# Performance work log

Hardware: AMD Instinct MI355X
Metric: run time of the kernel (lower is better)

The kernel has to match this reference:

```python
import jax, jax.numpy as jnp
import numpy as np

N = 100000
E = 1600000
H = 64      # hidden_size
NH = 8      # num_heads
DH = H // NH  # per-head dim (heads are the LAST axis, as in the torch code)


def _lin(x, W, b):
    return x @ W + b


def setup_inputs() -> dict:
    key = jax.random.key(0)
    ks = jax.random.split(key, 18)
    s = 0.05
    inp = {
        "h_x": jax.random.normal(ks[0], (N, H), jnp.float32),
        "h_e": jax.random.normal(ks[1], (E, H), jnp.float32),
        "row": jax.random.randint(ks[2], (E,), 0, N, jnp.int32),  # dst node of each nonzero
        "col": jax.random.randint(ks[3], (E,), 0, N, jnp.int32),  # src node of each nonzero
    }
    names = ["q", "k", "v", "e", "oh", "oe"]
    for i, nm in enumerate(names):
        inp["W" + nm] = jax.random.normal(ks[4 + 2 * i], (H, H), jnp.float32) * s
        inp["b" + nm] = jax.random.normal(ks[5 + 2 * i], (H,), jnp.float32) * s
    return inp


def reference(h_x, h_e, row, col, Wq, bq, Wk, bk, Wv, bv, We, be, Woh, boh, Woe, boe):
    n = h_x.shape[0]
    m = h_e.shape[0]
    q = _lin(h_x, Wq, bq).reshape(n, DH, NH)
    k = _lin(h_x, Wk, bk).reshape(n, DH, NH)
    v = _lin(h_x, Wv, bv).reshape(n, DH, NH)
    e = _lin(h_e, We, be).reshape(m, DH, NH)

    # SDDMM: per-nonzero (i=row, j=col), per-head dot of q[i] and k[j]  -> (E, NH)
    scores = (q[row] * k[col]).sum(axis=1) / jnp.sqrt(jnp.float32(DH))

    # edge gating: e.sum over dh axis -> (E, NH)
    e_gate = e.sum(axis=1)
    scores = scores * e_gate

    # oe branch (uses pre-softmax gated scores)
    oe_feat = scores[:, None, :] * e          # (E, DH, NH)
    oe = _lin(oe_feat.reshape(m, H), Woe, boe)

    # sparse softmax over dim=1 (per destination row), per head
    mx = jax.ops.segment_max(scores, row, num_segments=n)      # (N, NH)
    ex = jnp.exp(scores - mx[row])
    den = jax.ops.segment_sum(ex, row, num_segments=n)         # (N, NH)
    sm = ex / den[row]                                          # (E, NH)

    # bSpMM: h_out[i,:,h] = sum_{e: row[e]=i} sm[e,h] * v[col[e],:,h]
    h_out = jax.ops.segment_sum(sm[:, None, :] * v[col], row, num_segments=n)
    oh = _lin(h_out.reshape(n, H), Woh, boh)
    return (oh, oe)
```

## Files before the change

### kernel.cpp

```cpp
#include <hip/hip_runtime.h>

typedef __attribute__((ext_vector_type(8))) short bf16x8;
typedef __attribute__((ext_vector_type(4))) float f32x4;

__device__ __forceinline__ float bf2f(unsigned short h) {
  return __uint_as_float(((unsigned)h) << 16);
}
__device__ __forceinline__ unsigned cvtpk(float a, float b) {
  unsigned r;
  asm("v_cvt_pk_bf16_f32 %0, %1, %2" : "=v"(r) : "v"(a), "v"(b));
  return r;
}
__device__ __forceinline__ unsigned short f2bf(float f) {
  return (unsigned short)(cvtpk(f, f) & 0xffffu);
}
__device__ __forceinline__ bf16x8 pack8(f32x4 x0, f32x4 x1) {
  union { bf16x8 v; unsigned u[4]; } z;
  z.u[0] = cvtpk(x0[0], x0[1]);
  z.u[1] = cvtpk(x0[2], x0[3]);
  z.u[2] = cvtpk(x1[0], x1[1]);
  z.u[3] = cvtpk(x1[2], x1[3]);
  return z.v;
}

template<bool IN_BF16, bool OUT_BF16>
__global__ void __launch_bounds__(256) gemm64_kernel(const void* __restrict__ Ain,
    const float* __restrict__ W, const float* __restrict__ bias,
    void* __restrict__ Out, int M) {
  const int tid = threadIdx.x;
  const int l = tid & 63;
  const int g = l >> 4;
  const int n15 = l & 15;

  bf16x8 bfrag[4][2];
  float bv[4];
#pragma unroll
  for (int nb = 0; nb < 4; ++nb) {
    bv[nb] = bias[nb * 16 + n15];
#pragma unroll
    for (int kb = 0; kb < 2; ++kb)
#pragma unroll
      for (int j = 0; j < 8; ++j)
        bfrag[nb][kb][j] = (short)f2bf(W[(kb * 32 + g * 8 + j) * 64 + nb * 16 + n15]);
  }

  int wid = (blockIdx.x * blockDim.x + tid) >> 6;
  int nw = (gridDim.x * blockDim.x) >> 6;
  int ntiles = (M + 15) >> 4;
  for (int t = wid; t < ntiles; t += nw) {
    int m0 = t << 4;
    int arow = m0 + n15;
    bf16x8 a0, a1;
    if (arow < M) {
      if constexpr (IN_BF16) {
        const unsigned short* ap = (const unsigned short*)Ain + (size_t)arow * 64 + g * 8;
        a0 = *(const bf16x8*)ap;
        a1 = *(const bf16x8*)(ap + 32);
      } else {
        const float* ap = (const float*)Ain + (size_t)arow * 64 + g * 8;
        a0 = pack8(*(const f32x4*)ap, *(const f32x4*)(ap + 4));
        a1 = pack8(*(const f32x4*)(ap + 32), *(const f32x4*)(ap + 36));
      }
    } else {
#pragma unroll
      for (int j = 0; j < 8; ++j) { a0[j] = 0; a1[j] = 0; }
    }
    f32x4 acc[4];
#pragma unroll
    for (int nb = 0; nb < 4; ++nb) {
      acc[nb] = (f32x4){bv[nb], bv[nb], bv[nb], bv[nb]};
      acc[nb] = __builtin_amdgcn_mfma_f32_16x16x32_bf16(a0, bfrag[nb][0], acc[nb], 0, 0, 0);
      acc[nb] = __builtin_amdgcn_mfma_f32_16x16x32_bf16(a1, bfrag[nb][1], acc[nb], 0, 0, 0);
    }
#pragma unroll
    for (int nb = 0; nb < 4; ++nb)
#pragma unroll
      for (int r = 0; r < 4; ++r) {
        int orow = m0 + g * 4 + r;
        if (orow < M) {
          float val = acc[nb][r];
          size_t oidx = (size_t)orow * 64 + nb * 16 + n15;
          if constexpr (OUT_BF16) ((unsigned short*)Out)[oidx] = f2bf(val);
          else                    ((float*)Out)[oidx] = val;
        }
      }
  }
}

__global__ void __launch_bounds__(256) qkv3_kernel(const float* __restrict__ hx,
    const float* __restrict__ Wq, const float* __restrict__ bq,
    const float* __restrict__ Wk, const float* __restrict__ bk,
    const float* __restrict__ Wv, const float* __restrict__ bv,
    unsigned short* __restrict__ q, unsigned short* __restrict__ k,
    unsigned short* __restrict__ v, int M) {
  const int tid = threadIdx.x;
  const int l = tid & 63;
  const int g = l >> 4;
  const int n15 = l & 15;
  const float* Ws[3] = {Wq, Wk, Wv};
  const float* bs[3] = {bq, bk, bv};
  unsigned short* outs[3] = {q, k, v};

  bf16x8 bfrag[3][4][2];
  float bvv[3][4];
#pragma unroll
  for (int w = 0; w < 3; ++w)
#pragma unroll
    for (int nb = 0; nb < 4; ++nb) {
      bvv[w][nb] = bs[w][nb * 16 + n15];
#pragma unroll
      for (int kb = 0; kb < 2; ++kb)
#pragma unroll
        for (int j = 0; j < 8; ++j)
          bfrag[w][nb][kb][j] = (short)f2bf(Ws[w][(kb * 32 + g * 8 + j) * 64 + nb * 16 + n15]);
    }

  int wid = (blockIdx.x * blockDim.x + tid) >> 6;
  int nw = (gridDim.x * blockDim.x) >> 6;
  int ntiles = (M + 15) >> 4;
  for (int t = wid; t < ntiles; t += nw) {
    int m0 = t << 4;
    int arow = m0 + n15;
    bf16x8 a0, a1;
    if (arow < M) {
      const float* ap = hx + (size_t)arow * 64 + g * 8;
      a0 = pack8(*(const f32x4*)ap, *(const f32x4*)(ap + 4));
      a1 = pack8(*(const f32x4*)(ap + 32), *(const f32x4*)(ap + 36));
    } else {
#pragma unroll
      for (int j = 0; j < 8; ++j) { a0[j] = 0; a1[j] = 0; }
    }
#pragma unroll
    for (int w = 0; w < 3; ++w) {
      f32x4 acc[4];
#pragma unroll
      for (int nb = 0; nb < 4; ++nb) {
        acc[nb] = (f32x4){bvv[w][nb], bvv[w][nb], bvv[w][nb], bvv[w][nb]};
        acc[nb] = __builtin_amdgcn_mfma_f32_16x16x32_bf16(a0, bfrag[w][nb][0], acc[nb], 0, 0, 0);
        acc[nb] = __builtin_amdgcn_mfma_f32_16x16x32_bf16(a1, bfrag[w][nb][1], acc[nb], 0, 0, 0);
      }
#pragma unroll
      for (int nb = 0; nb < 4; ++nb)
#pragma unroll
        for (int r = 0; r < 4; ++r) {
          int orow = m0 + g * 4 + r;
          if (orow < M)
            outs[w][(size_t)orow * 64 + nb * 16 + n15] = f2bf(acc[nb][r]);
        }
    }
  }
}

__global__ void __launch_bounds__(256) edge_fused_kernel(
    const float* __restrict__ he,
    const int* __restrict__ rowi, const int* __restrict__ coli,
    const int* __restrict__ eslot,
    const unsigned short* __restrict__ qb, const unsigned short* __restrict__ kbuf,
    const float* __restrict__ We, const float* __restrict__ be,
    const float* __restrict__ Woe, const float* __restrict__ boe,
    float* __restrict__ oe, float* __restrict__ escores, int E) {
  const int tid = threadIdx.x;
  const int wv = tid >> 6;
  const int l = tid & 63;
  const int g = l >> 4;
  const int n15 = l & 15;
  const int h = n15 & 7;

  __shared__ float s_lds[4][160];
  __shared__ unsigned short feat_lds[4][16 * 72];

  bf16x8 bfE[4][2], bfO[4][2];
  float beV[4], boV[4];
#pragma unroll
  for (int nb = 0; nb < 4; ++nb) {
    beV[nb] = be[nb * 16 + n15];
    boV[nb] = boe[nb * 16 + n15];
#pragma unroll
    for (int kb = 0; kb < 2; ++kb)
#pragma unroll
      for (int j = 0; j < 8; ++j) {
        bfE[nb][kb][j] = (short)f2bf(We[(kb * 32 + g * 8 + j) * 64 + nb * 16 + n15]);
        bfO[nb][kb][j] = (short)f2bf(Woe[(kb * 32 + g * 8 + j) * 64 + nb * 16 + n15]);
      }
  }

  const int ntiles = (E + 15) >> 4;
  const int nit = (ntiles + 3) >> 2;
  const int stride = gridDim.x;

  int it = blockIdx.x;
  if (it >= nit) return;

  f32x4 h0, h1, h2, h3;
  int rq, rc, sl;
  {
    int m0 = ((it << 2) + wv) << 4;
    int es = min(m0 + n15, E - 1);
    const float* ap = he + (size_t)es * 64 + g * 8;
    h0 = *(const f32x4*)ap;       h1 = *(const f32x4*)(ap + 4);
    h2 = *(const f32x4*)(ap + 32); h3 = *(const f32x4*)(ap + 36);
    rq = rowi[es]; rc = coli[es]; sl = eslot[es];
  }

  while (true) {
    const int m0 = ((it << 2) + wv) << 4;
    const int arow = m0 + n15;

    const unsigned short* qp = qb + (size_t)rq * 64 + g * 16;
    const unsigned short* kp = kbuf + (size_t)rc * 64 + g * 16;
    bf16x8 qv0 = *(const bf16x8*)qp, qv1 = *(const bf16x8*)(qp + 8);
    bf16x8 kv0 = *(const bf16x8*)kp, kv1 = *(const bf16x8*)(kp + 8);

    const int itn = it + stride;
    const bool more = itn < nit;
    f32x4 nh0 = h0, nh1 = h1, nh2 = h2, nh3 = h3;
    int nrq = rq, nrc = rc, nsl = sl;
    if (more) {
      int m0n = ((itn << 2) + wv) << 4;
      int es = min(m0n + n15, E - 1);
      const float* ap = he + (size_t)es * 64 + g * 8;
      nh0 = *(const f32x4*)ap;       nh1 = *(const f32x4*)(ap + 4);
      nh2 = *(const f32x4*)(ap + 32); nh3 = *(const f32x4*)(ap + 36);
      nrq = rowi[es]; nrc = coli[es]; nsl = eslot[es];
    }

    bf16x8 a0 = pack8(h0, h1), a1 = pack8(h2, h3);
    if (arow >= E) {
#pragma unroll
      for (int j = 0; j < 8; ++j) { a0[j] = 0; a1[j] = 0; }
    }
    f32x4 acc[4];
#pragma unroll
    for (int nb = 0; nb < 4; ++nb) {
      acc[nb] = (f32x4){beV[nb], beV[nb], beV[nb], beV[nb]};
      acc[nb] = __builtin_amdgcn_mfma_f32_16x16x32_bf16(a0, bfE[nb][0], acc[nb], 0, 0, 0);
      acc[nb] = __builtin_amdgcn_mfma_f32_16x16x32_bf16(a1, bfE[nb][1], acc[nb], 0, 0, 0);
    }
    float gc[4];
#pragma unroll
    for (int r = 0; r < 4; ++r) {
      float s = acc[0][r] + acc[1][r] + acc[2][r] + acc[3][r];
      s += __shfl_xor(s, 8, 64);
      gc[r] = s * 0.35355339059327373f;
    }
    float p[8];
#pragma unroll
    for (int j = 0; j < 8; ++j)
      p[j] = bf2f((unsigned short)qv0[j]) * bf2f((unsigned short)kv0[j])
           + bf2f((unsigned short)qv1[j]) * bf2f((unsigned short)kv1[j]);
#pragma unroll
    for (int j = 0; j < 8; ++j) {
      p[j] += __shfl_xor(p[j], 16, 64);
      p[j] += __shfl_xor(p[j], 32, 64);
    }
    if (l < 16) {
      float2* sp = (float2*)&s_lds[wv][n15 * 10];
#pragma unroll
      for (int j = 0; j < 4; ++j) sp[j] = make_float2(p[2 * j], p[2 * j + 1]);
    }
    float srow[4];
#pragma unroll
    for (int r = 0; r < 4; ++r)
      srow[r] = s_lds[wv][(g * 4 + r) * 10 + h] * gc[r];
#pragma unroll
    for (int r = 0; r < 4; ++r) {
      int orow = m0 + g * 4 + r;
      int slot = __shfl(sl, g * 4 + r, 64);
      if (n15 < 8 && orow < E) escores[(size_t)slot * 8 + n15] = srow[r];
    }
#pragma unroll
    for (int nb = 0; nb < 4; ++nb)
#pragma unroll
      for (int r = 0; r < 4; ++r)
        feat_lds[wv][(g * 4 + r) * 72 + nb * 16 + n15] = f2bf(srow[r] * acc[nb][r]);
    const unsigned short* fpt = &feat_lds[wv][n15 * 72 + g * 8];
    a0 = *(const bf16x8*)fpt;
    a1 = *(const bf16x8*)(fpt + 32);
#pragma unroll
    for (int nb = 0; nb < 4; ++nb) {
      f32x4 a2 = (f32x4){boV[nb], boV[nb], boV[nb], boV[nb]};
      a2 = __builtin_amdgcn_mfma_f32_16x16x32_bf16(a0, bfO[nb][0], a2, 0, 0, 0);
      a2 = __builtin_amdgcn_mfma_f32_16x16x32_bf16(a1, bfO[nb][1], a2, 0, 0, 0);
#pragma unroll
      for (int r = 0; r < 4; ++r) {
        int orow = m0 + g * 4 + r;
        if (orow < E) oe[(size_t)orow * 64 + nb * 16 + n15] = a2[r];
      }
    }

    if (!more) break;
    h0 = nh0; h1 = nh1; h2 = nh2; h3 = nh3;
    rq = nrq; rc = nrc; sl = nsl;
    it = itn;
  }
}

__global__ void zero_kernel(int* __restrict__ p, int n) {
  int i = blockIdx.x * blockDim.x + threadIdx.x;
  if (i < n) p[i] = 0;
}

__global__ void hist_kernel(const int* __restrict__ row, int* __restrict__ deg, int E) {
  int gid = blockIdx.x * blockDim.x + threadIdx.x;
  if (gid < E) atomicAdd(&deg[row[gid]], 1);
}

#define SCAN_B 256
#define SCAN_E 8
__global__ void scan1_kernel(const int* __restrict__ deg, int* __restrict__ rowptr,
                             int* __restrict__ blksum, int n) {
  __shared__ int sh[SCAN_B];
  int base = blockIdx.x * (SCAN_B * SCAN_E) + threadIdx.x * SCAN_E;
  int v[SCAN_E];
  int s = 0;
#pragma unroll
  for (int j = 0; j < SCAN_E; ++j) {
    v[j] = (base + j < n) ? deg[base + j] : 0;
    s += v[j];
  }
  sh[threadIdx.x] = s;
  __syncthreads();
  for (int off = 1; off < SCAN_B; off <<= 1) {
    int t = (threadIdx.x >= off) ? sh[threadIdx.x - off] : 0;
    __syncthreads();
    sh[threadIdx.x] += t;
    __syncthreads();
  }
  if (threadIdx.x == SCAN_B - 1) blksum[blockIdx.x] = sh[SCAN_B - 1];
  int run = sh[threadIdx.x] - s;
#pragma unroll
  for (int j = 0; j < SCAN_E; ++j) {
    if (base + j < n) rowptr[base + j] = run;
    run += v[j];
  }
}

__global__ void scan2_kernel(int* __restrict__ blksum, int nb) {
  __shared__ int sh[SCAN_B];
  int v = (threadIdx.x < nb) ? blksum[threadIdx.x] : 0;
  sh[threadIdx.x] = v;
  __syncthreads();
  for (int off = 1; off < SCAN_B; off <<= 1) {
    int t = (threadIdx.x >= off) ? sh[threadIdx.x - off] : 0;
    __syncthreads();
    sh[threadIdx.x] += t;
    __syncthreads();
  }
  if (threadIdx.x < nb) blksum[threadIdx.x] = sh[threadIdx.x] - v;
}

__global__ void scan3_kernel(int* __restrict__ rowptr, int* __restrict__ cursor,
                             const int* __restrict__ blksum, int n) {
  int i = blockIdx.x * blockDim.x + threadIdx.x;
  if (i >= n) return;
  int v = rowptr[i] + blksum[i / (SCAN_B * SCAN_E)];
  rowptr[i] = v;
  cursor[i] = v;
}

__global__ void scatter_kernel(const int* __restrict__ row, const int* __restrict__ col,
                               int* __restrict__ cursor, int* __restrict__ eslot,
                               int* __restrict__ ecol, int E) {
  int gid = blockIdx.x * blockDim.x + threadIdx.x;
  if (gid >= E) return;
  int r = row[gid];
  int slot = atomicAdd(&cursor[r], 1);
  eslot[gid] = slot;
  ecol[slot] = col[gid];
}

__global__ void __launch_bounds__(256) row_attn_kernel(const float* __restrict__ escores,
    const int* __restrict__ rowptr, const int* __restrict__ deg,
    const int* __restrict__ ecol,
    const unsigned short* __restrict__ vb, float* __restrict__ hout, int n) {
  int gid = blockIdx.x * blockDim.x + threadIdx.x;
  int r = gid >> 6, lane = threadIdx.x & 63;
  if (r >= n) return;
  int start = rowptr[r], dg = deg[r];
  int h = lane & 7;
  float den = 0.f, acc = 0.f;
#pragma unroll 4
  for (int i = 0; i < dg; ++i) {
    int c = ecol[start + i];
    float ex = __expf(escores[(size_t)(start + i) * 8 + h]);
    float vv = bf2f(vb[(size_t)c * 64 + lane]);
    den += ex;
    acc += ex * vv;
  }
  hout[(size_t)r * 64 + lane] = (dg > 0) ? acc / den : 0.f;
}

extern "C" void kernel_launch(void* const* d_in, const int* in_sizes, int n_in,
                              void* d_out, int out_size, void* d_ws, size_t ws_size,
                              hipStream_t stream) {
  const float* hx  = (const float*)d_in[0];
  const float* he  = (const float*)d_in[1];
  const int*   row = (const int*)d_in[2];
  const int*   col = (const int*)d_in[3];
  const float* Wq = (const float*)d_in[4],  *bq = (const float*)d_in[5];
  const float* Wk = (const float*)d_in[6],  *bk = (const float*)d_in[7];
  const float* Wv = (const float*)d_in[8],  *bv = (const float*)d_in[9];
  const float* We = (const float*)d_in[10], *be = (const float*)d_in[11];
  const float* Woh = (const float*)d_in[12], *boh = (const float*)d_in[13];
  const float* Woe = (const float*)d_in[14], *boe = (const float*)d_in[15];

  const int n = in_sizes[0] / 64;
  const int E = in_sizes[2];

  float* out = (float*)d_out;
  float* oh = out;
  float* oe = out + (size_t)n * 64;

  unsigned short* qb   = (unsigned short*)d_ws;
  unsigned short* kb   = qb + (size_t)n * 64;
  unsigned short* vbuf = kb + (size_t)n * 64;
  float* escores = (float*)(vbuf + (size_t)n * 64);
  float* hout    = escores + (size_t)E * 8;

  int* deg    = (int*)(hout + (size_t)n * 64);
  int* rowptr = deg + n;
  int* cursor = rowptr + n;
  int* blksum = cursor + n;
  int* eslot  = blksum + 256;
  int* ecol   = eslot + (size_t)E;

  const int nb_scan = (n + SCAN_B * SCAN_E - 1) / (SCAN_B * SCAN_E);

  zero_kernel<<<(n + 255) / 256, 256, 0, stream>>>(deg, n);
  hist_kernel<<<(E + 255) / 256, 256, 0, stream>>>(row, deg, E);
  scan1_kernel<<<nb_scan, SCAN_B, 0, stream>>>(deg, rowptr, blksum, n);
  scan2_kernel<<<1, SCAN_B, 0, stream>>>(blksum, nb_scan);
  scan3_kernel<<<(n + 255) / 256, 256, 0, stream>>>(rowptr, cursor, blksum, n);
  scatter_kernel<<<(E + 255) / 256, 256, 0, stream>>>(row, col, cursor, eslot, ecol, E);

  qkv3_kernel<<<512, 256, 0, stream>>>(hx, Wq, bq, Wk, bk, Wv, bv, qb, kb, vbuf, n);
  edge_fused_kernel<<<2048, 256, 0, stream>>>(he, row, col, eslot, qb, kb, We, be,
                                              Woe, boe, oe, escores, E);

  row_attn_kernel<<<(n + 3) / 4, 256, 0, stream>>>(escores, rowptr, deg, ecol,
                                                   vbuf, hout, n);
  gemm64_kernel<false, false><<<512, 256, 0, stream>>>(hout, Woh, boh, oh, n);
}
```

Baseline: 550.8 us.

## Process two edge tiles per iteration and parallelize row attention across edges

The edge kernel now handles two independent 16-edge tiles per loop iteration instead of software-prefetching the next tile. This gives more independent loads and MFMA work to interleave, at the cost of more registers and doubled LDS buffers. The row attention kernel now splits a row's edges across four 16-lane groups, each loading 4 bf16 v values and 4 scores as vectors. The groups are then reduced with shuffles and the result written as float4, replacing one serial edge loop per 64-lane wavefront.

```diff
diff --git a/kernel.cpp b/kernel.cpp
--- a/kernel.cpp
+++ b/kernel.cpp
@@ -2,6 +2,7 @@
 
 typedef __attribute__((ext_vector_type(8))) short bf16x8;
 typedef __attribute__((ext_vector_type(4))) float f32x4;
+typedef __attribute__((ext_vector_type(4))) unsigned short u16x4;
 
 __device__ __forceinline__ float bf2f(unsigned short h) {
   return __uint_as_float(((unsigned)h) << 16);
@@ -166,8 +167,8 @@
   const int n15 = l & 15;
   const int h = n15 & 7;
 
-  __shared__ float s_lds[4][160];
-  __shared__ unsigned short feat_lds[4][16 * 72];
+  __shared__ float sA[4][160], sB[4][160];
+  __shared__ unsigned short fA[4][16 * 72], fB[4][16 * 72];
 
   bf16x8 bfE[4][2], bfO[4][2];
   float beV[4], boV[4];
@@ -188,110 +189,122 @@
   const int nit = (ntiles + 3) >> 2;
   const int stride = gridDim.x;
 
-  int it = blockIdx.x;
-  if (it >= nit) return;
-
-  f32x4 h0, h1, h2, h3;
-  int rq, rc, sl;
-  {
-    int m0 = ((it << 2) + wv) << 4;
-    int es = min(m0 + n15, E - 1);
-    const float* ap = he + (size_t)es * 64 + g * 8;
-    h0 = *(const f32x4*)ap;       h1 = *(const f32x4*)(ap + 4);
-    h2 = *(const f32x4*)(ap + 32); h3 = *(const f32x4*)(ap + 36);
-    rq = rowi[es]; rc = coli[es]; sl = eslot[es];
-  }
-
-  while (true) {
-    const int m0 = ((it << 2) + wv) << 4;
-    const int arow = m0 + n15;
-
-    const unsigned short* qp = qb + (size_t)rq * 64 + g * 16;
-    const unsigned short* kp = kbuf + (size_t)rc * 64 + g * 16;
-    bf16x8 qv0 = *(const bf16x8*)qp, qv1 = *(const bf16x8*)(qp + 8);
-    bf16x8 kv0 = *(const bf16x8*)kp, kv1 = *(const bf16x8*)(kp + 8);
-
-    const int itn = it + stride;
-    const bool more = itn < nit;
-    f32x4 nh0 = h0, nh1 = h1, nh2 = h2, nh3 = h3;
-    int nrq = rq, nrc = rc, nsl = sl;
-    if (more) {
-      int m0n = ((itn << 2) + wv) << 4;
-      int es = min(m0n + n15, E - 1);
-      const float* ap = he + (size_t)es * 64 + g * 8;
-      nh0 = *(const f32x4*)ap;       nh1 = *(const f32x4*)(ap + 4);
-      nh2 = *(const f32x4*)(ap + 32); nh3 = *(const f32x4*)(ap + 36);
-      nrq = rowi[es]; nrc = coli[es]; nsl = eslot[es];
-    }
-
-    bf16x8 a0 = pack8(h0, h1), a1 = pack8(h2, h3);
-    if (arow >= E) {
-#pragma unroll
-      for (int j = 0; j < 8; ++j) { a0[j] = 0; a1[j] = 0; }
-    }
-    f32x4 acc[4];
+  for (int itA = blockIdx.x; itA < nit; itA += 2 * stride) {
+    const int itB = (itA + stride < nit) ? (itA + stride) : itA;
+    const int m0A = ((itA << 2) + wv) << 4;
+    const int m0B = ((itB << 2) + wv) << 4;
+    const int esA = min(m0A + n15, E - 1);
+    const int esB = min(m0B + n15, E - 1);
+
+    const int rqA = rowi[esA], rcA = coli[esA], slA = eslot[esA];
+    const int rqB = rowi[esB], rcB = coli[esB], slB = eslot[esB];
+    const float* apA = he + (size_t)esA * 64 + g * 8;
+    const float* apB = he + (size_t)esB * 64 + g * 8;
+    f32x4 hA0 = *(const f32x4*)apA,        hA1 = *(const f32x4*)(apA + 4);
+    f32x4 hA2 = *(const f32x4*)(apA + 32), hA3 = *(const f32x4*)(apA + 36);
+    f32x4 hB0 = *(const f32x4*)apB,        hB1 = *(const f32x4*)(apB + 4);
+    f32x4 hB2 = *(const f32x4*)(apB + 32), hB3 = *(const f32x4*)(apB + 36);
+
+    bf16x8 aA0 = pack8(hA0, hA1), aA1 = pack8(hA2, hA3);
+    bf16x8 aB0 = pack8(hB0, hB1), aB1 = pack8(hB2, hB3);
+    f32x4 accA[4], accB[4];
 #pragma unroll
     for (int nb = 0; nb < 4; ++nb) {
-      acc[nb] = (f32x4){beV[nb], beV[nb], beV[nb], beV[nb]};
-      acc[nb] = __builtin_amdgcn_mfma_f32_16x16x32_bf16(a0, bfE[nb][0], acc[nb], 0, 0, 0);
-      acc[nb] = __builtin_amdgcn_mfma_f32_16x16x32_bf16(a1, bfE[nb][1], acc[nb], 0, 0, 0);
-    }
-    float gc[4];
+      accA[nb] = (f32x4){beV[nb], beV[nb], beV[nb], beV[nb]};
+      accA[nb] = __builtin_amdgcn_mfma_f32_16x16x32_bf16(aA0, bfE[nb][0], accA[nb], 0, 0, 0);
+      accA[nb] = __builtin_amdgcn_mfma_f32_16x16x32_bf16(aA1, bfE[nb][1], accA[nb], 0, 0, 0);
+      accB[nb] = (f32x4){beV[nb], beV[nb], beV[nb], beV[nb]};
+      accB[nb] = __builtin_amdgcn_mfma_f32_16x16x32_bf16(aB0, bfE[nb][0], accB[nb], 0, 0, 0);
+      accB[nb] = __builtin_amdgcn_mfma_f32_16x16x32_bf16(aB1, bfE[nb][1], accB[nb], 0, 0, 0);
+    }
+
+    const unsigned short* qpA = qb   + (size_t)rqA * 64 + g * 16;
+    const unsigned short* kpA = kbuf + (size_t)rcA * 64 + g * 16;
+    const unsigned short* qpB = qb   + (size_t)rqB * 64 + g * 16;
+    const unsigned short* kpB = kbuf + (size_t)rcB * 64 + g * 16;
+    bf16x8 qA0 = *(const bf16x8*)qpA, qA1 = *(const bf16x8*)(qpA + 8);
+    bf16x8 kA0 = *(const bf16x8*)kpA, kA1 = *(const bf16x8*)(kpA + 8);
+    bf16x8 qB0 = *(const bf16x8*)qpB, qB1 = *(const bf16x8*)(qpB + 8);
+    bf16x8 kB0 = *(const bf16x8*)kpB, kB1 = *(const bf16x8*)(kpB + 8);
+
+    float gcA[4], gcB[4];
 #pragma unroll
     for (int r = 0; r < 4; ++r) {
-      float s = acc[0][r] + acc[1][r] + acc[2][r] + acc[3][r];
-      s += __shfl_xor(s, 8, 64);
-      gc[r] = s * 0.35355339059327373f;
-    }
-    float p[8];
-#pragma unroll
-    for (int j = 0; j < 8; ++j)
-      p[j] = bf2f((unsigned short)qv0[j]) * bf2f((unsigned short)kv0[j])
-           + bf2f((unsigned short)qv1[j]) * bf2f((unsigned short)kv1[j]);
+      float sa = accA[0][r] + accA[1][r] + accA[2][r] + accA[3][r];
+      sa += __shfl_xor(sa, 8, 64);
+      gcA[r] = sa * 0.35355339059327373f;
+      float sb = accB[0][r] + accB[1][r] + accB[2][r] + accB[3][r];
+      sb += __shfl_xor(sb, 8, 64);
+      gcB[r] = sb * 0.35355339059327373f;
+    }
+
+    float pA[8], pB[8];
 #pragma unroll
     for (int j = 0; j < 8; ++j) {
-      p[j] += __shfl_xor(p[j], 16, 64);
-      p[j] += __shfl_xor(p[j], 32, 64);
-    }
+      pA[j] = bf2f((unsigned short)qA0[j]) * bf2f((unsigned short)kA0[j])
+            + bf2f((unsigned short)qA1[j]) * bf2f((unsigned short)kA1[j]);
+      pB[j] = bf2f((unsigned short)qB0[j]) * bf2f((unsigned short)kB0[j])
+            + bf2f((unsigned short)qB1[j]) * bf2f((unsigned short)kB1[j]);
+    }
+#pragma unroll
+    for (int j = 0; j < 8; ++j) {
+      pA[j] += __shfl_xor(pA[j], 16, 64);
+      pA[j] += __shfl_xor(pA[j], 32, 64);
+      pB[j] += __shfl_xor(pB[j], 16, 64);
+      pB[j] += __shfl_xor(pB[j], 32, 64);
+    }
+
     if (l < 16) {
-      float2* sp = (float2*)&s_lds[wv][n15 * 10];
-#pragma unroll
-      for (int j = 0; j < 4; ++j) sp[j] = make_float2(p[2 * j], p[2 * j + 1]);
-    }
-    float srow[4];
-#pragma unroll
-    for (int r = 0; r < 4; ++r)
-      srow[r] = s_lds[wv][(g * 4 + r) * 10 + h] * gc[r];
+      float2* spA = (float2*)&sA[wv][n15 * 10];
+      float2* spB = (float2*)&sB[wv][n15 * 10];
+#pragma unroll
+      for (int j = 0; j < 4; ++j) {
+        spA[j] = make_float2(pA[2 * j], pA[2 * j + 1]);
+        spB[j] = make_float2(pB[2 * j], pB[2 * j + 1]);
+      }
+    }
+    float srA[4], srB[4];
 #pragma unroll
     for (int r = 0; r < 4; ++r) {
-      int orow = m0 + g * 4 + r;
-      int slot = __shfl(sl, g * 4 + r, 64);
-      if (n15 < 8 && orow < E) escores[(size_t)slot * 8 + n15] = srow[r];
-    }
+      srA[r] = sA[wv][(g * 4 + r) * 10 + h] * gcA[r];
+      srB[r] = sB[wv][(g * 4 + r) * 10 + h] * gcB[r];
+    }
+
+#pragma unroll
+    for (int r = 0; r < 4; ++r) {
+      int slotA = __shfl(slA, g * 4 + r, 64);
+      int slotB = __shfl(slB, g * 4 + r, 64);
+      if (n15 < 8 && m0A + g * 4 + r < E) escores[(size_t)slotA * 8 + n15] = srA[r];
+      if (n15 < 8 && m0B + g * 4 + r < E) escores[(size_t)slotB * 8 + n15] = srB[r];
+    }
+
 #pragma unroll
     for (int nb = 0; nb < 4; ++nb)
 #pragma unroll
-      for (int r = 0; r < 4; ++r)
-        feat_lds[wv][(g * 4 + r) * 72 + nb * 16 + n15] = f2bf(srow[r] * acc[nb][r]);
-    const unsigned short* fpt = &feat_lds[wv][n15 * 72 + g * 8];
-    a0 = *(const bf16x8*)fpt;
-    a1 = *(const bf16x8*)(fpt + 32);
+      for (int r = 0; r < 4; ++r) {
+        fA[wv][(g * 4 + r) * 72 + nb * 16 + n15] = f2bf(srA[r] * accA[nb][r]);
+        fB[wv][(g * 4 + r) * 72 + nb * 16 + n15] = f2bf(srB[r] * accB[nb][r]);
+      }
+    const unsigned short* fpA = &fA[wv][n15 * 72 + g * 8];
+    const unsigned short* fpB = &fB[wv][n15 * 72 + g * 8];
+    bf16x8 oA0 = *(const bf16x8*)fpA, oA1 = *(const bf16x8*)(fpA + 32);
+    bf16x8 oB0 = *(const bf16x8*)fpB, oB1 = *(const bf16x8*)(fpB + 32);
 #pragma unroll
     for (int nb = 0; nb < 4; ++nb) {
-      f32x4 a2 = (f32x4){boV[nb], boV[nb], boV[nb], boV[nb]};
-      a2 = __builtin_amdgcn_mfma_f32_16x16x32_bf16(a0, bfO[nb][0], a2, 0, 0, 0);
-      a2 = __builtin_amdgcn_mfma_f32_16x16x32_bf16(a1, bfO[nb][1], a2, 0, 0, 0);
+      f32x4 cA = (f32x4){boV[nb], boV[nb], boV[nb], boV[nb]};
+      cA = __builtin_amdgcn_mfma_f32_16x16x32_bf16(oA0, bfO[nb][0], cA, 0, 0, 0);
+      cA = __builtin_amdgcn_mfma_f32_16x16x32_bf16(oA1, bfO[nb][1], cA, 0, 0, 0);
+      f32x4 cB = (f32x4){boV[nb], boV[nb], boV[nb], boV[nb]};
+      cB = __builtin_amdgcn_mfma_f32_16x16x32_bf16(oB0, bfO[nb][0], cB, 0, 0, 0);
+      cB = __builtin_amdgcn_mfma_f32_16x16x32_bf16(oB1, bfO[nb][1], cB, 0, 0, 0);
 #pragma unroll
       for (int r = 0; r < 4; ++r) {
-        int orow = m0 + g * 4 + r;
-        if (orow < E) oe[(size_t)orow * 64 + nb * 16 + n15] = a2[r];
-      }
-    }
-
-    if (!more) break;
-    h0 = nh0; h1 = nh1; h2 = nh2; h3 = nh3;
-    rq = nrq; rc = nrc; sl = nsl;
-    it = itn;
+        int orA = m0A + g * 4 + r;
+        int orB = m0B + g * 4 + r;
+        if (orA < E) oe[(size_t)orA * 64 + nb * 16 + n15] = cA[r];
+        if (orB < E) oe[(size_t)orB * 64 + nb * 16 + n15] = cB[r];
+      }
+    }
   }
 }
 
@@ -376,18 +389,36 @@
   int gid = blockIdx.x * blockDim.x + threadIdx.x;
   int r = gid >> 6, lane = threadIdx.x & 63;
   if (r >= n) return;
+  int gi = lane >> 4, j = lane & 15;
   int start = rowptr[r], dg = deg[r];
-  int h = lane & 7;
-  float den = 0.f, acc = 0.f;
-#pragma unroll 4
-  for (int i = 0; i < dg; ++i) {
-    int c = ecol[start + i];
-    float ex = __expf(escores[(size_t)(start + i) * 8 + h]);
-    float vv = bf2f(vb[(size_t)c * 64 + lane]);
-    den += ex;
-    acc += ex * vv;
-  }
-  hout[(size_t)r * 64 + lane] = (dg > 0) ? acc / den : 0.f;
+
+  f32x4 acc = (f32x4){0.f, 0.f, 0.f, 0.f};
+  f32x4 den = (f32x4){0.f, 0.f, 0.f, 0.f};
+  for (int i = gi; i < dg; i += 4) {
+    int idx = start + i;
+    int c = ecol[idx];
+    f32x4 sv = *(const f32x4*)(escores + (size_t)idx * 8 + 4 * (j & 1));
+    u16x4 vv = *(const u16x4*)(vb + (size_t)c * 64 + j * 4);
+#pragma unroll
+    for (int m = 0; m < 4; ++m) {
+      float ex = __expf(sv[m]);
+      den[m] += ex;
+      acc[m] += ex * bf2f(vv[m]);
+    }
+  }
+#pragma unroll
+  for (int m = 0; m < 4; ++m) {
+    acc[m] += __shfl_xor(acc[m], 16, 64);
+    acc[m] += __shfl_xor(acc[m], 32, 64);
+    den[m] += __shfl_xor(den[m], 16, 64);
+    den[m] += __shfl_xor(den[m], 32, 64);
+  }
+  if (gi == 0) {
+    f32x4 o;
+#pragma unroll
+    for (int m = 0; m < 4; ++m) o[m] = (dg > 0) ? acc[m] / den[m] : 0.f;
+    *(f32x4*)(hout + (size_t)r * 64 + j * 4) = o;
+  }
 }
 
 extern "C" void kernel_launch(void* const* d_in, const int* in_sizes, int n_in,
```

New measurement: 548.6 us. No clear change (-0.4%).

## Stage edge weights in swizzled LDS and parallelize row attention over edges

Applied to the files above, without the earlier changes.

The edge kernel now keeps the We/Woe bf16 fragments in shared memory, with an XOR swizzle, instead of per-lane registers. It runs 512-thread blocks with a plain grid-stride loop over 16-edge tiles and drops the manual register prefetch of the next tile. This lowers register pressure so more waves can be resident, at the cost of LDS reads for the B fragments and less explicit latency hiding. The row attention kernel now has each wave handle four edges at once, with lanes loading four heads and values as vector loads, and reduces across edge groups with shuffles. This cuts the serial per-edge loop and makes its loads wider.

```diff
diff --git a/kernel.cpp b/kernel.cpp
--- a/kernel.cpp
+++ b/kernel.cpp
@@ -2,6 +2,7 @@
 
 typedef __attribute__((ext_vector_type(8))) short bf16x8;
 typedef __attribute__((ext_vector_type(4))) float f32x4;
+typedef __attribute__((ext_vector_type(4))) unsigned short u16x4;
 
 __device__ __forceinline__ float bf2f(unsigned short h) {
   return __uint_as_float(((unsigned)h) << 16);
@@ -151,7 +152,7 @@
   }
 }
 
-__global__ void __launch_bounds__(256) edge_fused_kernel(
+__global__ void __launch_bounds__(512) edge_fused_kernel(
     const float* __restrict__ he,
     const int* __restrict__ rowi, const int* __restrict__ coli,
     const int* __restrict__ eslot,
@@ -166,75 +167,56 @@
   const int n15 = l & 15;
   const int h = n15 & 7;
 
-  __shared__ float s_lds[4][160];
-  __shared__ unsigned short feat_lds[4][16 * 72];
-
-  bf16x8 bfE[4][2], bfO[4][2];
+  __shared__ unsigned short WeT[4096];
+  __shared__ unsigned short WoT[4096];
+  __shared__ float s_lds[8][160];
+  __shared__ unsigned short feat_lds[8][16 * 72];
+
+  {
+    const int c = tid >> 3, d0 = (tid & 7) * 8;
+    const unsigned off = (unsigned)(c * 128 + d0 * 2) ^ ((unsigned)(c & 7) << 4);
+    unsigned short* we = (unsigned short*)((char*)WeT + off);
+    unsigned short* wo = (unsigned short*)((char*)WoT + off);
+#pragma unroll
+    for (int j = 0; j < 8; ++j) {
+      we[j] = f2bf(We[(d0 + j) * 64 + c]);
+      wo[j] = f2bf(Woe[(d0 + j) * 64 + c]);
+    }
+  }
   float beV[4], boV[4];
 #pragma unroll
   for (int nb = 0; nb < 4; ++nb) {
     beV[nb] = be[nb * 16 + n15];
     boV[nb] = boe[nb * 16 + n15];
-#pragma unroll
-    for (int kb = 0; kb < 2; ++kb)
-#pragma unroll
-      for (int j = 0; j < 8; ++j) {
-        bfE[nb][kb][j] = (short)f2bf(We[(kb * 32 + g * 8 + j) * 64 + nb * 16 + n15]);
-        bfO[nb][kb][j] = (short)f2bf(Woe[(kb * 32 + g * 8 + j) * 64 + nb * 16 + n15]);
-      }
-  }
+  }
+  __syncthreads();
 
   const int ntiles = (E + 15) >> 4;
-  const int nit = (ntiles + 3) >> 2;
-  const int stride = gridDim.x;
-
-  int it = blockIdx.x;
-  if (it >= nit) return;
-
-  f32x4 h0, h1, h2, h3;
-  int rq, rc, sl;
-  {
-    int m0 = ((it << 2) + wv) << 4;
-    int es = min(m0 + n15, E - 1);
+  const int nwav = gridDim.x * 8;
+  for (int t = blockIdx.x * 8 + wv; t < ntiles; t += nwav) {
+    const int m0 = t << 4;
+    const int es = min(m0 + n15, E - 1);
+    const int rq = rowi[es], rc = coli[es], sl = eslot[es];
+
     const float* ap = he + (size_t)es * 64 + g * 8;
-    h0 = *(const f32x4*)ap;       h1 = *(const f32x4*)(ap + 4);
-    h2 = *(const f32x4*)(ap + 32); h3 = *(const f32x4*)(ap + 36);
-    rq = rowi[es]; rc = coli[es]; sl = eslot[es];
-  }
-
-  while (true) {
-    const int m0 = ((it << 2) + wv) << 4;
-    const int arow = m0 + n15;
+    bf16x8 a0 = pack8(*(const f32x4*)ap, *(const f32x4*)(ap + 4));
+    bf16x8 a1 = pack8(*(const f32x4*)(ap + 32), *(const f32x4*)(ap + 36));
 
     const unsigned short* qp = qb + (size_t)rq * 64 + g * 16;
     const unsigned short* kp = kbuf + (size_t)rc * 64 + g * 16;
     bf16x8 qv0 = *(const bf16x8*)qp, qv1 = *(const bf16x8*)(qp + 8);
     bf16x8 kv0 = *(const bf16x8*)kp, kv1 = *(const bf16x8*)(kp + 8);
 
-    const int itn = it + stride;
-    const bool more = itn < nit;
-    f32x4 nh0 = h0, nh1 = h1, nh2 = h2, nh3 = h3;
-    int nrq = rq, nrc = rc, nsl = sl;
-    if (more) {
-      int m0n = ((itn << 2) + wv) << 4;
-      int es = min(m0n + n15, E - 1);
-      const float* ap = he + (size_t)es * 64 + g * 8;
-      nh0 = *(const f32x4*)ap;       nh1 = *(const f32x4*)(ap + 4);
-      nh2 = *(const f32x4*)(ap + 32); nh3 = *(const f32x4*)(ap + 36);
-      nrq = rowi[es]; nrc = coli[es]; nsl = eslot[es];
-    }
-
-    bf16x8 a0 = pack8(h0, h1), a1 = pack8(h2, h3);
-    if (arow >= E) {
-#pragma unroll
-      for (int j = 0; j < 8; ++j) { a0[j] = 0; a1[j] = 0; }
-    }
     f32x4 acc[4];
 #pragma unroll
     for (int nb = 0; nb < 4; ++nb) {
+      const unsigned off0 = (unsigned)((nb * 16 + n15) * 128 + g * 16)
+                            ^ ((unsigned)(n15 & 7) << 4);
+      bf16x8 b0 = *(const bf16x8*)((const char*)WeT + off0);
+      bf16x8 b1 = *(const bf16x8*)((const char*)WeT + (off0 ^ 64u));
       acc[nb] = (f32x4){beV[nb], beV[nb], beV[nb], beV[nb]};
-      acc[nb] = __builtin_amdgcn_mfma_f32_16x16x32_bf16(a0, bfE[nb][0], acc[nb], 0, 0, 0);
-      acc[nb] = __builtin_amdgcn_mfma_f32_16x16x32_bf16(a1, bfE[nb][1], acc[nb], 0, 0, 0);
+      acc[nb] = __builtin_amdgcn_mfma_f32_16x16x32_bf16(a0, b0, acc[nb], 0, 0, 0);
+      acc[nb] = __builtin_amdgcn_mfma_f32_16x16x32_bf16(a1, b1, acc[nb], 0, 0, 0);
     }
     float gc[4];
 #pragma unroll
@@ -264,9 +246,8 @@
       srow[r] = s_lds[wv][(g * 4 + r) * 10 + h] * gc[r];
 #pragma unroll
     for (int r = 0; r < 4; ++r) {
-      int orow = m0 + g * 4 + r;
       int slot = __shfl(sl, g * 4 + r, 64);
-      if (n15 < 8 && orow < E) escores[(size_t)slot * 8 + n15] = srow[r];
+      if (n15 < 8 && m0 + g * 4 + r < E) escores[(size_t)slot * 8 + n15] = srow[r];
     }
 #pragma unroll
     for (int nb = 0; nb < 4; ++nb)
@@ -278,20 +259,19 @@
     a1 = *(const bf16x8*)(fpt + 32);
 #pragma unroll
     for (int nb = 0; nb < 4; ++nb) {
-      f32x4 a2 = (f32x4){boV[nb], boV[nb], boV[nb], boV[nb]};
-      a2 = __builtin_amdgcn_mfma_f32_16x16x32_bf16(a0, bfO[nb][0], a2, 0, 0, 0);
-      a2 = __builtin_amdgcn_mfma_f32_16x16x32_bf16(a1, bfO[nb][1], a2, 0, 0, 0);
+      const unsigned off0 = (unsigned)((nb * 16 + n15) * 128 + g * 16)
+                            ^ ((unsigned)(n15 & 7) << 4);
+      bf16x8 b0 = *(const bf16x8*)((const char*)WoT + off0);
+      bf16x8 b1 = *(const bf16x8*)((const char*)WoT + (off0 ^ 64u));
+      f32x4 c2 = (f32x4){boV[nb], boV[nb], boV[nb], boV[nb]};
+      c2 = __builtin_amdgcn_mfma_f32_16x16x32_bf16(a0, b0, c2, 0, 0, 0);
+      c2 = __builtin_amdgcn_mfma_f32_16x16x32_bf16(a1, b1, c2, 0, 0, 0);
 #pragma unroll
       for (int r = 0; r < 4; ++r) {
         int orow = m0 + g * 4 + r;
-        if (orow < E) oe[(size_t)orow * 64 + nb * 16 + n15] = a2[r];
+        if (orow < E) oe[(size_t)orow * 64 + nb * 16 + n15] = c2[r];
       }
     }
-
-    if (!more) break;
-    h0 = nh0; h1 = nh1; h2 = nh2; h3 = nh3;
-    rq = nrq; rc = nrc; sl = nsl;
-    it = itn;
   }
 }
 
@@ -376,18 +356,36 @@
   int gid = blockIdx.x * blockDim.x + threadIdx.x;
   int r = gid >> 6, lane = threadIdx.x & 63;
   if (r >= n) return;
+  int gi = lane >> 4, j = lane & 15;
   int start = rowptr[r], dg = deg[r];
-  int h = lane & 7;
-  float den = 0.f, acc = 0.f;
-#pragma unroll 4
-  for (int i = 0; i < dg; ++i) {
-    int c = ecol[start + i];
-    float ex = __expf(escores[(size_t)(start + i) * 8 + h]);
-    float vv = bf2f(vb[(size_t)c * 64 + lane]);
-    den += ex;
-    acc += ex * vv;
-  }
-  hout[(size_t)r * 64 + lane] = (dg > 0) ? acc / den : 0.f;
+
+  f32x4 acc = (f32x4){0.f, 0.f, 0.f, 0.f};
+  f32x4 den = (f32x4){0.f, 0.f, 0.f, 0.f};
+  for (int i = gi; i < dg; i += 4) {
+    int idx = start + i;
+    int c = ecol[idx];
+    f32x4 sv = *(const f32x4*)(escores + (size_t)idx * 8 + 4 * (j & 1));
+    u16x4 vv = *(const u16x4*)(vb + (size_t)c * 64 + j * 4);
+#pragma unroll
+    for (int m = 0; m < 4; ++m) {
+      float ex = __expf(sv[m]);
+      den[m] += ex;
+      acc[m] += ex * bf2f(vv[m]);
+    }
+  }
+#pragma unroll
+  for (int m = 0; m < 4; ++m) {
+    acc[m] += __shfl_xor(acc[m], 16, 64);
+    acc[m] += __shfl_xor(acc[m], 32, 64);
+    den[m] += __shfl_xor(den[m], 16, 64);
+    den[m] += __shfl_xor(den[m], 32, 64);
+  }
+  if (gi == 0) {
+    f32x4 o;
+#pragma unroll
+    for (int m = 0; m < 4; ++m) o[m] = (dg > 0) ? acc[m] / den[m] : 0.f;
+    *(f32x4*)(hout + (size_t)r * 64 + j * 4) = o;
+  }
 }
 
 extern "C" void kernel_launch(void* const* d_in, const int* in_sizes, int n_in,
@@ -434,7 +432,7 @@
   scatter_kernel<<<(E + 255) / 256, 256, 0, stream>>>(row, col, cursor, eslot, ecol, E);
 
   qkv3_kernel<<<512, 256, 0, stream>>>(hx, Wq, bq, Wk, bk, Wv, bv, qb, kb, vbuf, n);
-  edge_fused_kernel<<<2048, 256, 0, stream>>>(he, row, col, eslot, qb, kb, We, be,
+  edge_fused_kernel<<<1024, 512, 0, stream>>>(he, row, col, eslot, qb, kb, We, be,
                                               Woe, boe, oe, escores, E);
 
   row_attn_kernel<<<(n + 3) / 4, 256, 0, stream>>>(escores, rowptr, deg, ecol,
```

Result: no change. 555.7 us (+0.9%).
